# Optimization experiments

Hardware: AMD Instinct MI355X
Metric: run time of the kernel (lower is better)

## Reference

```python
import jax, jax.numpy as jnp
import numpy as np

LEVELS = 256          # 8-bit fake quant, quant_levels=256 in forward
SLM_CUTOFF = 0.05     # lower bound of the SLM LUT (file-loaded in original)
EPS = 1e-8


def _stats(t, pct):
    # QuantizeStats first-calibration-step semantics:
    # max = percentile(t, pct); min = t.min() if >= 0 else -max
    mx = jnp.percentile(t, pct)
    mn = jnp.min(t)
    mn = jnp.where(mn >= 0.0, mn, -mx)
    return jax.lax.stop_gradient(mn), jax.lax.stop_gradient(mx)


def _fake_quant_det(x, mn, mx, lut_min=None):
    diff = mx - mn
    q = jnp.clip(x, mn, mx)
    q = (q - mn) / (diff + EPS) * (LEVELS - 1)
    q = jnp.round(q) / (LEVELS - 1) * diff + mn
    if lut_min is not None:
        # clip positive part up to lut_min*max, negative part down to -lut_min*|min|
        pos = jax.nn.relu(q)
        neg = q - pos
        lms_p = lut_min * mx
        pos = jnp.where(pos < lms_p, lms_p, pos)
        lms_n = lut_min * jnp.abs(mn)
        neg = jnp.where(neg > -lms_n, -lms_n, neg)
        q = pos + neg
    # straight-through estimator (QuantizeValue.backward passes grad through)
    return x + jax.lax.stop_gradient(q - x)


def _fake_quant_rand(x, mn, mx, key):
    diff = mx - mn
    q = jnp.clip(x, mn, mx)
    q = (q - mn) / (diff + EPS) * (LEVELS - 1)
    noise = jax.random.uniform(key, q.shape, q.dtype) - 0.5  # stochastic rounding
    q = jnp.round(q + noise) / (LEVELS - 1) * diff + mn
    return x + jax.lax.stop_gradient(q - x)


def setup_inputs() -> dict:
    key = jax.random.key(0)
    kx, ky = jax.random.split(key)
    x = jax.random.normal(kx, (2, 4, 2048, 64), dtype=jnp.float32)
    y = jax.random.normal(ky, (2, 4, 64, 2048), dtype=jnp.float32)
    return {"x": x, "y": y}


def reference(x, y):
    # QuantizedMatmul.forward, quantize=True, training path
    x_min, x_max = _stats(x, 99.99)
    y_min, y_max = _stats(y, 98.0)
    xq = _fake_quant_det(x, x_min, x_max)
    yq = _fake_quant_det(y, y_min, y_max, SLM_CUTOFF)
    out = jnp.matmul(xq, yq)           # [B,H,M,N]
    o_min, o_max = _stats(out, 99.9999)
    return _fake_quant_rand(out, o_min, o_max, jax.random.key(1))
```

## Files before the change

### kernel.cpp

```cpp
#include <hip/hip_runtime.h>
#include <math.h>

#define CAP  (1u<<20)
#define LCAP 12288
#define LBUF 4096

typedef __attribute__((ext_vector_type(4))) float f32x4;
typedef __attribute__((ext_vector_type(8))) __bf16 bf16x8;
typedef __attribute__((ext_vector_type(8))) unsigned short u16x8;
typedef __attribute__((ext_vector_type(4))) unsigned short u16x4;

__device__ __forceinline__ unsigned f2key(float f){
  unsigned u = __float_as_uint(f);
  return (u & 0x80000000u) ? ~u : (u | 0x80000000u);
}
__device__ __forceinline__ float key2f(unsigned k){
  unsigned u = (k & 0x80000000u) ? (k & 0x7fffffffu) : ~k;
  return __uint_as_float(u);
}
__device__ __forceinline__ unsigned short f2bf(float f){
  unsigned u = __float_as_uint(f);
  u += 0x7FFFu + ((u>>16)&1u);
  return (unsigned short)(u>>16);
}

__device__ __forceinline__ void stage_bf16_tiles(
    const unsigned short* __restrict__ xq, const unsigned short* __restrict__ yqT,
    unsigned short* As, unsigned short* Bs, int brow, int bcol, int tid){
  #pragma unroll
  for (int i=0;i<4;i++){
    int u = tid + i*256;
    int row = u >> 3, ko = (u & 7) << 3;
    u16x8 v = *(const u16x8*)&xq[(size_t)(brow+row)*64 + ko];
    unsigned slot = ((unsigned)(ko>>3)) ^ ((unsigned)row & 7u);
    *(u16x8*)&As[(unsigned)row*64u + slot*8u] = v;
  }
  #pragma unroll
  for (int i=0;i<4;i++){
    int u = tid + i*256;
    int col = u >> 3, ko = (u & 7) << 3;
    u16x8 v = *(const u16x8*)&yqT[(size_t)(bcol+col)*64 + ko];
    unsigned slot = ((unsigned)(ko>>3)) ^ ((unsigned)col & 7u);
    *(u16x8*)&Bs[(unsigned)col*64u + slot*8u] = v;
  }
}

__device__ __forceinline__ void mfma_tile(
    const unsigned short* As, const unsigned short* Bs,
    f32x4 acc[2][8], int w, int lr, int lg){
  #pragma unroll
  for (int kk=0; kk<2; ++kk){
    bf16x8 a[2], bb[8];
    #pragma unroll
    for (int rt=0;rt<2;rt++){
      int row = w*32 + rt*16 + lr;
      unsigned slot = (unsigned)(kk*4 + lg) ^ ((unsigned)row & 7u);
      a[rt] = __builtin_bit_cast(bf16x8, *(const u16x8*)&As[(unsigned)row*64u + slot*8u]);
    }
    #pragma unroll
    for (int ct=0;ct<8;ct++){
      int col = ct*16 + lr;
      unsigned slot = (unsigned)(kk*4 + lg) ^ ((unsigned)col & 7u);
      bb[ct] = __builtin_bit_cast(bf16x8, *(const u16x8*)&Bs[(unsigned)col*64u + slot*8u]);
    }
    #pragma unroll
    for (int rt=0;rt<2;rt++)
      #pragma unroll
      for (int ct=0;ct<8;ct++)
        acc[rt][ct] = __builtin_amdgcn_mfma_f32_16x16x32_bf16(a[rt], bb[ct], acc[rt][ct], 0, 0, 0);
  }
}

__global__ void init_kernel(unsigned* ctrl){
  int tid = blockIdx.x*blockDim.x + threadIdx.x;
  int stride = gridDim.x*blockDim.x;
  for (int i=tid;i<8192;i+=stride) ctrl[i]=0u;
  if (tid<16) ctrl[12291+tid]=0u;
  if (tid>=16 && tid<19) ctrl[12288+(tid-16)]=0xFFFFFFFFu;
}

__global__ __launch_bounds__(256) void hist2_kernel(
    const float4* __restrict__ dA, const float4* __restrict__ dB, int n4A, int n4B,
    unsigned* __restrict__ hA, unsigned* __restrict__ hB,
    unsigned* __restrict__ mkA, unsigned* __restrict__ mkB){
  const int z = blockIdx.y;
  const float4* __restrict__ data = z ? dB : dA;
  const int n4 = z ? n4B : n4A;
  unsigned* hist = z ? hB : hA;
  unsigned* minKey = z ? mkB : mkA;
  __shared__ unsigned sh[8*4096];
  int tid = threadIdx.x;
  for (int i=tid;i<8*4096;i+=blockDim.x) sh[i]=0u;
  __syncthreads();
  const unsigned p = (unsigned)(tid & 7);
  const unsigned cp = p << 12;
  const unsigned rot = p << 2;
  unsigned lmin=0xFFFFFFFFu;
  int idx = blockIdx.x*blockDim.x + tid;
  int stride = gridDim.x*blockDim.x;
  for (int i=idx;i<n4;i+=stride){
    float4 v = data[i];
    unsigned k0=f2key(v.x), k1=f2key(v.y), k2=f2key(v.z), k3=f2key(v.w);
    atomicAdd(&sh[cp + (((k0>>20)+rot)&4095u)],1u);
    atomicAdd(&sh[cp + (((k1>>20)+rot)&4095u)],1u);
    atomicAdd(&sh[cp + (((k2>>20)+rot)&4095u)],1u);
    atomicAdd(&sh[cp + (((k3>>20)+rot)&4095u)],1u);
    lmin = min(lmin, min(min(k0,k1),min(k2,k3)));
  }
  #pragma unroll
  for (int off=32; off; off>>=1) lmin = min(lmin, __shfl_xor(lmin, off));
  if ((tid&63)==0) atomicMin(minKey, lmin);
  __syncthreads();
  for (int i=tid;i<4096;i+=blockDim.x){
    unsigned c=0;
    #pragma unroll
    for (int q=0;q<8;q++) c += sh[(q<<12) + (((unsigned)i + (q<<2))&4095u)];
    if(c) atomicAdd(&hist[i],c);
  }
}

__global__ __launch_bounds__(256) void collect2_kernel(
    const float4* __restrict__ dA, const float4* __restrict__ dB, int n4A, int n4B,
    const unsigned* __restrict__ hA, const unsigned* __restrict__ hB,
    unsigned k1A, unsigned k2A, unsigned k1B, unsigned k2B,
    float* __restrict__ candA, float* __restrict__ candB,
    unsigned* __restrict__ cntA, unsigned* __restrict__ cntB){
  const int z = blockIdx.y;
  const float4* __restrict__ data = z ? dB : dA;
  const int n4 = z ? n4B : n4A;
  const unsigned* __restrict__ hist = z ? hB : hA;
  const unsigned k1 = z ? k1B : k1A;
  const unsigned k2 = z ? k2B : k2A;
  float* cand = z ? candB : candA;
  unsigned* cnt = z ? cntB : cntA;
  __shared__ float sc[LBUF];
  __shared__ unsigned part[256];
  __shared__ unsigned sBi[2];
  __shared__ unsigned scnt, sbase;
  const int t = threadIdx.x;
  if (t==0) scnt=0u;
  unsigned h[16]; unsigned s=0;
  #pragma unroll
  for (int i=0;i<16;i++){ h[i] = hist[t*16+i]; s += h[i]; }
  part[t] = s;
  __syncthreads();
  for (int off=1; off<256; off<<=1){
    unsigned add = (t+off<256) ? part[t+off] : 0u;
    __syncthreads();
    part[t] += add;
    __syncthreads();
  }
  unsigned cum = (t<255) ? part[t+1] : 0u;
  for (int i=15;i>=0;--i){
    unsigned hh = h[i];
    unsigned b = (unsigned)(t*16+i);
    if (cum < k1 && cum + hh >= k1){ sBi[1] = b; }
    if (cum < k2 && cum + hh >= k2){ sBi[0] = b; }
    cum += hh;
  }
  __syncthreads();
  const unsigned blo = sBi[0], bhi = sBi[1];
  int idx = blockIdx.x*blockDim.x + t;
  int stride = gridDim.x*blockDim.x;
  for (int i=idx;i<n4;i+=stride){
    float4 v = data[i];
    float r[4] = {v.x,v.y,v.z,v.w};
    #pragma unroll
    for (int j=0;j<4;j++){
      unsigned b = f2key(r[j]) >> 20;
      if (b>=blo && b<=bhi){
        unsigned p = atomicAdd(&scnt,1u);
        if (p < LBUF) sc[p] = r[j];
        else { unsigned g = atomicAdd(cnt,1u); if (g<CAP) cand[g]=r[j]; }
      }
    }
  }
  __syncthreads();
  unsigned c = scnt; if (c > LBUF) c = LBUF;
  if (t==0 && c>0) sbase = atomicAdd(cnt, c);
  __syncthreads();
  for (unsigned i=t; i<c; i+=256){
    unsigned g = sbase + i;
    if (g < CAP) cand[g] = sc[i];
  }
}

__global__ __launch_bounds__(1024) void select2_kernel(
    const float* __restrict__ candA, const float* __restrict__ candB,
    const unsigned* __restrict__ cntA, const unsigned* __restrict__ cntB,
    const unsigned* __restrict__ hA, const unsigned* __restrict__ hB,
    const unsigned* __restrict__ mkA, const unsigned* __restrict__ mkB,
    unsigned k1A, unsigned k2A, unsigned k1B, unsigned k2B,
    double fracA, double fracB,
    float* __restrict__ stA, float* __restrict__ stB){
  const int z = blockIdx.x;
  const float* __restrict__ cand = z ? candB : candA;
  const unsigned* cnt = z ? cntB : cntA;
  const unsigned* __restrict__ hist_g = z ? hB : hA;
  const unsigned* mk  = z ? mkB  : mkA;
  const unsigned k1 = z ? k1B : k1A;
  const unsigned k2 = z ? k2B : k2A;
  const double frac = z ? fracB : fracA;
  float* stats = z ? stB : stA;

  __shared__ unsigned keys[LCAP];
  __shared__ unsigned histP[16*258];
  __shared__ unsigned hist[256];
  __shared__ unsigned part[256];
  __shared__ unsigned sAbove;
  __shared__ unsigned sPrefix, sK;
  __shared__ unsigned sKey[2];
  const int t = threadIdx.x;
  unsigned m = *cnt; if (m > CAP) m = CAP;
  for (unsigned i=t; i<m && i<LCAP; i+=1024) keys[i] = f2key(cand[i]);

  if (t==0) sAbove = 0u;
  if (hist_g){
    unsigned h[16]; unsigned s=0;
    if (t<256){
      #pragma unroll
      for (int i=0;i<16;i++){ h[i] = hist_g[t*16+i]; s += h[i]; }
      part[t] = s;
    }
    __syncthreads();
    for (int off=1; off<256; off<<=1){
      unsigned add = (t<256 && t+off<256) ? part[t+off] : 0u;
      __syncthreads();
      if (t<256) part[t] += add;
      __syncthreads();
    }
    if (t<256){
      unsigned cum = (t<255) ? part[t+1] : 0u;
      for (int i=15;i>=0;--i){
        unsigned hh = h[i];
        if (cum < k1 && cum + hh >= k1){ sAbove = cum; }
        cum += hh;
      }
    }
  }
  __syncthreads();
  const unsigned above = sAbove;

  for (int tg=0; tg<2; ++tg){
    unsigned k = ((tg==0) ? k1 : k2) - above;
    unsigned prefix = 0u, pmask = 0u;
    for (int s=24; s>=0; s-=8){
      for (int i=t;i<16*258;i+=1024) histP[i]=0u;
      __syncthreads();
      const unsigned base = (unsigned)(t & 15) * 258u;
      for (unsigned i=t;i<m;i+=1024){
        unsigned key = (i<LCAP) ? keys[i] : f2key(cand[i]);
        if ((key & pmask) == prefix) atomicAdd(&histP[base + ((key>>s)&255u)],1u);
      }
      __syncthreads();
      if (t<256){
        unsigned c=0;
        #pragma unroll
        for (int q=0;q<16;q++) c += histP[(unsigned)q*258u + (unsigned)t];
        hist[t] = c;
      }
      __syncthreads();
      if (t<64){
        unsigned h0=hist[t*4+0], h1=hist[t*4+1], h2=hist[t*4+2], h3=hist[t*4+3];
        unsigned g = h0+h1+h2+h3;
        unsigned acc = g;
        #pragma unroll
        for (int off=1; off<64; off<<=1){
          unsigned v = __shfl_down(acc, off);
          acc += (t+off<64) ? v : 0u;
        }
        unsigned ca3 = acc - g;
        unsigned ca2 = ca3 + h3;
        unsigned ca1 = ca2 + h2;
        unsigned ca0 = ca1 + h1;
        if (ca3<k && ca3+h3>=k){ sPrefix = prefix | ((unsigned)(4*t+3)<<s); sK = k-ca3; }
        if (ca2<k && ca2+h2>=k){ sPrefix = prefix | ((unsigned)(4*t+2)<<s); sK = k-ca2; }
        if (ca1<k && ca1+h1>=k){ sPrefix = prefix | ((unsigned)(4*t+1)<<s); sK = k-ca1; }
        if (ca0<k && ca0+h0>=k){ sPrefix = prefix | ((unsigned)(4*t+0)<<s); sK = k-ca0; }
      }
      __syncthreads();
      prefix = sPrefix;
      pmask |= (255u << s);
      k = sK;
    }
    if (t==0) sKey[tg] = prefix;
    __syncthreads();
  }
  if (t==0){
    float vhi = key2f(sKey[0]);
    float vlo = key2f(sKey[1]);
    double mx = (double)vlo + frac * ((double)vhi - (double)vlo);
    float mxf = (float)mx;
    float mnraw = key2f(*mk);
    float mnf = (mnraw >= 0.0f) ? mnraw : -mxf;
    stats[0]=mnf; stats[1]=mxf;
  }
}

__global__ __launch_bounds__(256) void prep_quant_kernel(
    const float4* __restrict__ x, const float* __restrict__ y,
    unsigned short* __restrict__ xq, unsigned short* __restrict__ yqT,
    int n4x, const float* __restrict__ stA, const float* __restrict__ stB){
  if (blockIdx.y == 0){
    const float amn=stA[0], amx=stA[1];
    const float adiff=amx-amn, adenom=adiff+1e-8f;
    int idx = blockIdx.x*256 + threadIdx.x;
    int stride = gridDim.x*256;
    for (int i=idx; i<n4x; i+=stride){
      float4 v = x[i];
      float rr[4]={v.x,v.y,v.z,v.w};
      u16x4 qv;
      #pragma unroll
      for (int j=0;j<4;j++){
        float xv = rr[j];
        float q = fminf(fmaxf(xv, amn), amx);
        q = (q - amn) / adenom * 255.0f;
        q = rintf(q);
        q = q / 255.0f * adiff + amn;
        qv[j] = f2bf(xv + (q - xv));
      }
      *(u16x4*)&xq[(size_t)i*4] = qv;
    }
  } else {
    __shared__ unsigned short Ys[64*72];
    const float bmn=stB[0], bmx=stB[1];
    const float bdiff=bmx-bmn, bdenom=bdiff+1e-8f;
    const float blp=0.05f*bmx, bln=0.05f*fabsf(bmn);
    const int blk = blockIdx.x;
    const int b = blk >> 5, ctile = blk & 31;
    const float* Y = y + (size_t)b*64*2048 + ctile*64;
    const int t = threadIdx.x;
    #pragma unroll
    for (int i=0;i<4;i++){
      int u = t + i*256;
      int k = u >> 4;
      int c4 = (u & 15) << 2;
      float4 v = *(const float4*)&Y[(size_t)k*2048 + c4];
      float rr[4]={v.x,v.y,v.z,v.w};
      #pragma unroll
      for (int j=0;j<4;j++){
        float xv = rr[j];
        float q = fminf(fmaxf(xv, bmn), bmx);
        q = (q - bmn) / bdenom * 255.0f;
        q = rintf(q);
        q = q / 255.0f * bdiff + bmn;
        float pos = fmaxf(q, 0.0f);
        float neg = q - pos;
        pos = (pos < blp) ? blp : pos;
        neg = (neg > -bln) ? -bln : neg;
        q = pos + neg;
        Ys[(c4+j)*72 + k] = f2bf(xv + (q - xv));
      }
    }
    __syncthreads();
    #pragma unroll
    for (int i=0;i<2;i++){
      int u = t + i*256;
      int col = u >> 3, ko = (u & 7) << 3;
      u16x8 v = *(const u16x8*)&Ys[col*72 + ko];
      *(u16x8*)&yqT[((size_t)b*2048 + ctile*64 + col)*64 + ko] = v;
    }
  }
}

__global__ __launch_bounds__(256) void matmul_stats_kernel(
    const unsigned short* __restrict__ xq, const unsigned short* __restrict__ yqT,
    unsigned* __restrict__ bMaxKey, unsigned* __restrict__ bMinKey){
  __shared__ unsigned short As[128*64];
  __shared__ unsigned short Bs[128*64];
  __shared__ float wred[8];
  const int b = blockIdx.z;
  const unsigned short* xqb  = xq  + (size_t)b*2048*64;
  const unsigned short* yqTb = yqT + (size_t)b*2048*64;
  const int brow = blockIdx.y*128, bcol = blockIdx.x*128;
  const int tid = threadIdx.x;
  stage_bf16_tiles(xqb, yqTb, As, Bs, brow, bcol, tid);
  __syncthreads();
  const int w = tid >> 6, l = tid & 63, lr = l & 15, lg = l >> 4;
  f32x4 zero = {0.f,0.f,0.f,0.f};
  f32x4 acc[2][8];
  #pragma unroll
  for (int rt=0;rt<2;rt++)
    #pragma unroll
    for (int ct=0;ct<8;ct++) acc[rt][ct]=zero;
  mfma_tile(As, Bs, acc, w, lr, lg);
  float tmx = -3.4e38f, tmn = 3.4e38f;
  #pragma unroll
  for (int rt=0;rt<2;rt++)
    #pragma unroll
    for (int ct=0;ct<8;ct++)
      #pragma unroll
      for (int g=0; g<4; g++){
        float v = acc[rt][ct][g];
        tmx = fmaxf(tmx, v);
        tmn = fminf(tmn, v);
      }
  #pragma unroll
  for (int off=32; off; off>>=1){
    tmx = fmaxf(tmx, __shfl_xor(tmx, off));
    tmn = fminf(tmn, __shfl_xor(tmn, off));
  }
  if ((tid&63)==0){ wred[tid>>6]=tmx; wred[4+(tid>>6)]=tmn; }
  __syncthreads();
  if (tid==0){
    float m4 = fmaxf(fmaxf(wred[0],wred[1]),fmaxf(wred[2],wred[3]));
    float n4 = fminf(fminf(wred[4],wred[5]),fminf(wred[6],wred[7]));
    int bid = blockIdx.x + (blockIdx.y<<4) + (blockIdx.z<<8);
    bMaxKey[bid] = f2key(m4);
    bMinKey[bid] = f2key(n4);
  }
}

__global__ __launch_bounds__(256) void thresh_kernel(
    const unsigned* __restrict__ bMaxKey, const unsigned* __restrict__ bMinKey,
    unsigned kth, unsigned* __restrict__ tkey, unsigned* __restrict__ minKeyO){
  __shared__ unsigned red[8];
  const int t = threadIdx.x;
  unsigned kz[8];
  unsigned mn = 0xFFFFFFFFu;
  #pragma unroll
  for (int i=0;i<8;i++){ kz[i] = bMaxKey[t*8+i]; mn = min(mn, bMinKey[t*8+i]); }
  #pragma unroll
  for (int off=32; off; off>>=1) mn = min(mn, __shfl_xor(mn, off));
  if ((t&63)==0) red[4+(t>>6)] = mn;
  __syncthreads();
  if (t==0) *minKeyO = min(min(red[4],red[5]),min(red[6],red[7]));
  unsigned lo=0u, hi=0xFFFFFFFFu;
  while (lo < hi){
    unsigned mid = lo + ((hi-lo)>>1) + 1u;
    unsigned c = 0;
    #pragma unroll
    for (int i=0;i<8;i++) c += (kz[i] >= mid) ? 1u : 0u;
    #pragma unroll
    for (int off=32; off; off>>=1) c += __shfl_xor(c, off);
    __syncthreads();
    if ((t&63)==0) red[t>>6] = c;
    __syncthreads();
    unsigned tot = red[0]+red[1]+red[2]+red[3];
    if (tot >= kth) lo = mid; else hi = mid - 1u;
  }
  if (t==0) *tkey = lo;
}

__global__ __launch_bounds__(256) void collect_tile_kernel(
    const unsigned short* __restrict__ xq, const unsigned short* __restrict__ yqT,
    const unsigned* __restrict__ bMaxKey, const unsigned* __restrict__ tkey,
    float* __restrict__ cand, unsigned* __restrict__ cnt){
  const unsigned T = *tkey;
  const int bid = blockIdx.x + (blockIdx.y<<4) + (blockIdx.z<<8);
  if (bMaxKey[bid] < T) return;
  __shared__ unsigned short As[128*64];
  __shared__ unsigned short Bs[128*64];
  __shared__ float sc[LBUF];
  __shared__ unsigned scnt, sbase;
  const int b = blockIdx.z;
  const unsigned short* xqb  = xq  + (size_t)b*2048*64;
  const unsigned short* yqTb = yqT + (size_t)b*2048*64;
  const int brow = blockIdx.y*128, bcol = blockIdx.x*128;
  const int tid = threadIdx.x;
  if (tid==0) scnt=0u;
  stage_bf16_tiles(xqb, yqTb, As, Bs, brow, bcol, tid);
  __syncthreads();
  const int w = tid >> 6, l = tid & 63, lr = l & 15, lg = l >> 4;
  f32x4 zero = {0.f,0.f,0.f,0.f};
  f32x4 acc[2][8];
  #pragma unroll
  for (int rt=0;rt<2;rt++)
    #pragma unroll
    for (int ct=0;ct<8;ct++) acc[rt][ct]=zero;
  mfma_tile(As, Bs, acc, w, lr, lg);
  #pragma unroll
  for (int rt=0;rt<2;rt++)
    #pragma unroll
    for (int ct=0;ct<8;ct++)
      #pragma unroll
      for (int g=0; g<4; g++){
        float v = acc[rt][ct][g];
        if (f2key(v) >= T){
          unsigned p = atomicAdd(&scnt,1u);
          if (p < LBUF) sc[p] = v;
          else { unsigned gg = atomicAdd(cnt,1u); if (gg<CAP) cand[gg]=v; }
        }
      }
  __syncthreads();
  unsigned c = scnt; if (c > LBUF) c = LBUF;
  if (tid==0 && c>0) sbase = atomicAdd(cnt, c);
  __syncthreads();
  for (unsigned i=tid; i<c; i+=256){
    unsigned g = sbase + i;
    if (g < CAP) cand[g] = sc[i];
  }
}

__global__ __launch_bounds__(256) void matmul_quant_kernel(
    const unsigned short* __restrict__ xq, const unsigned short* __restrict__ yqT,
    float* __restrict__ C, const float* __restrict__ stO){
  __shared__ float smem[8704];
  unsigned short* As = (unsigned short*)smem;
  unsigned short* Bs = As + 8192;
  const float omn=stO[0], omx=stO[1];
  const float odiff=omx-omn, odenom=odiff+1e-8f;
  const int b = blockIdx.z;
  const unsigned short* xqb  = xq  + (size_t)b*2048*64;
  const unsigned short* yqTb = yqT + (size_t)b*2048*64;
  C += (size_t)b*2048*2048;
  const int brow = blockIdx.y*128, bcol = blockIdx.x*128;
  const int tid = threadIdx.x;
  stage_bf16_tiles(xqb, yqTb, As, Bs, brow, bcol, tid);
  __syncthreads();
  const int w = tid >> 6, l = tid & 63, lr = l & 15, lg = l >> 4;
  f32x4 zero = {0.f,0.f,0.f,0.f};
  f32x4 acc[2][8];
  #pragma unroll
  for (int rt=0;rt<2;rt++)
    #pragma unroll
    for (int ct=0;ct<8;ct++) acc[rt][ct]=zero;
  mfma_tile(As, Bs, acc, w, lr, lg);
  __syncthreads();
  float* Cw = smem + w*2176;
  #pragma unroll
  for (int h=0; h<2; ++h){
    #pragma unroll
    for (int rt=0;rt<2;rt++)
      #pragma unroll
      for (int c2=0;c2<4;c2++){
        int ct = h*4 + c2;
        #pragma unroll
        for (int g=0; g<4; g++){
          float x = acc[rt][ct][g];
          float q = fminf(fmaxf(x, omn), omx);
          q = (q - omn) / odenom * 255.0f;
          q = rintf(q);
          q = q / 255.0f * odiff + omn;
          Cw[(rt*16 + lg*4 + g)*68 + c2*16 + lr] = x + (q - x);
        }
      }
    #pragma unroll
    for (int i=0;i<8;i++){
      int u = l + 64*i;
      int row = u >> 4;
      int c4 = (u & 15) << 2;
      float4 v4 = *(float4*)&Cw[row*68 + c4];
      int gr = brow + w*32 + row;
      *(float4*)&C[(size_t)gr*2048 + bcol + h*64 + c4] = v4;
    }
  }
}

static void percentile_ranks(long long n, double pct, unsigned& k1, unsigned& k2, double& frac){
  double p = (double)(n - 1) * (pct / 100.0);
  double fi = floor(p);
  frac = p - fi;
  long long i0 = (long long)fi;
  k2 = (unsigned)(n - i0);
  k1 = k2 - 1u;
}

extern "C" void kernel_launch(void* const* d_in, const int* in_sizes, int n_in,
                              void* d_out, int out_size, void* d_ws, size_t ws_size,
                              hipStream_t stream) {
  const float* x = (const float*)d_in[0];
  const float* y = (const float*)d_in[1];
  float* out = (float*)d_out;
  char* ws = (char*)d_ws;

  const long long nX = (long long)in_sizes[0];
  const long long nY = (long long)in_sizes[1];
  const long long nO = (long long)out_size;
  const int nX4 = (int)(nX/4), nY4 = (int)(nY/4);

  float*    candx = (float*)(ws);
  float*    candy = (float*)(ws + (5ll<<20));
  float*    cando = (float*)(ws + (10ll<<20));
  unsigned* ctrl  = (unsigned*)(ws + (15ll<<20));
  unsigned short* xq  = (unsigned short*)(ws + (16ll<<20));
  unsigned short* yqT = (unsigned short*)(ws + (18ll<<20));
  unsigned *hx = ctrl, *hy = ctrl+4096;
  unsigned* minkey = ctrl + 12288;
  unsigned* cnt    = ctrl + 12291;
  unsigned* tkey   = ctrl + 12303;
  float* stx = (float*)(ctrl + 12304);
  float* sty = stx + 2;
  float* sto = stx + 4;
  unsigned* bMaxKey = ctrl + 12320;
  unsigned* bMinKey = ctrl + 14368;

  unsigned k1x,k2x,k1y,k2y,k1o,k2o; double fx,fy,fo;
  percentile_ranks(nX, 99.99,   k1x, k2x, fx);
  percentile_ranks(nY, 98.0,    k1y, k2y, fy);
  percentile_ranks(nO, 99.9999, k1o, k2o, fo);

  init_kernel<<<32,256,0,stream>>>(ctrl);

  hist2_kernel<<<dim3(128,2),256,0,stream>>>((const float4*)x,(const float4*)y,nX4,nY4,hx,hy,minkey+0,minkey+1);
  collect2_kernel<<<dim3(128,2),256,0,stream>>>((const float4*)x,(const float4*)y,nX4,nY4,hx,hy,
                                                k1x,k2x,k1y,k2y,candx,candy,cnt+0,cnt+1);
  select2_kernel<<<2,1024,0,stream>>>(candx,candy,cnt+0,cnt+1,hx,hy,minkey+0,minkey+1,
                                      k1x,k2x,k1y,k2y,fx,fy,stx,sty);

  prep_quant_kernel<<<dim3(256,2),256,0,stream>>>((const float4*)x, y, xq, yqT, nX4, stx, sty);

  matmul_stats_kernel<<<dim3(16,16,8),256,0,stream>>>(xq, yqT, bMaxKey, bMinKey);

  thresh_kernel<<<1,256,0,stream>>>(bMaxKey, bMinKey, k2o, tkey, minkey+2);
  collect_tile_kernel<<<dim3(16,16,8),256,0,stream>>>(xq, yqT, bMaxKey, tkey, cando, cnt+2);
  select2_kernel<<<1,1024,0,stream>>>(cando,cando,cnt+2,cnt+2,(const unsigned*)nullptr,(const unsigned*)nullptr,
                                      minkey+2,minkey+2,k1o,k2o,k1o,k2o,fo,fo,sto,sto);

  matmul_quant_kernel<<<dim3(16,16,8),256,0,stream>>>(xq, yqT, out, sto);
}
```

Baseline: 138.9 us.

## Fold threshold and output select into last-block tails of matmul kernels

The separate thresh_kernel and output select2_kernel launches are removed. Their work now runs in the last block to finish matmul_stats_kernel and collect_tile_kernel, detected with a global done counter and threadfence plus atomic loads. Candidates are stored as sortable keys, and the radix select runs in 256 threads inside the collect kernel. The final quant epilogue also drops its LDS transpose and writes scalars straight to global memory. This saves two kernel launches, but the tail work runs serially in a single block, and the uncoalesced stores may cost bandwidth. The select2 hist_g null check is also removed, so that path now always reads hist_g.

Result: slower. 206.2 us (+48.4%).

```diff
diff --git a/kernel.cpp b/kernel.cpp
--- a/kernel.cpp
+++ b/kernel.cpp
@@ -23,6 +23,7 @@
   u += 0x7FFFu + ((u>>16)&1u);
   return (unsigned short)(u>>16);
 }
+__device__ __forceinline__ unsigned aload(unsigned* p){ return atomicOr(p, 0u); }
 
 __device__ __forceinline__ void stage_bf16_tiles(
     const unsigned short* __restrict__ xq, const unsigned short* __restrict__ yqT,
@@ -215,7 +216,7 @@
   for (unsigned i=t; i<m && i<LCAP; i+=1024) keys[i] = f2key(cand[i]);
 
   if (t==0) sAbove = 0u;
-  if (hist_g){
+  {
     unsigned h[16]; unsigned s=0;
     if (t<256){
       #pragma unroll
@@ -365,10 +366,13 @@
 
 __global__ __launch_bounds__(256) void matmul_stats_kernel(
     const unsigned short* __restrict__ xq, const unsigned short* __restrict__ yqT,
-    unsigned* __restrict__ bMaxKey, unsigned* __restrict__ bMinKey){
+    unsigned* bMaxKey, unsigned* bMinKey,
+    unsigned* doneS, unsigned kth, unsigned* tkey, unsigned* minKeyO){
   __shared__ unsigned short As[128*64];
   __shared__ unsigned short Bs[128*64];
   __shared__ float wred[8];
+  __shared__ unsigned red[8];
+  __shared__ int sLast;
   const int b = blockIdx.z;
   const unsigned short* xqb  = xq  + (size_t)b*2048*64;
   const unsigned short* yqTb = yqT + (size_t)b*2048*64;
@@ -406,98 +410,173 @@
     float m4 = fmaxf(fmaxf(wred[0],wred[1]),fmaxf(wred[2],wred[3]));
     float n4 = fminf(fminf(wred[4],wred[5]),fminf(wred[6],wred[7]));
     int bid = blockIdx.x + (blockIdx.y<<4) + (blockIdx.z<<8);
-    bMaxKey[bid] = f2key(m4);
-    bMinKey[bid] = f2key(n4);
-  }
-}
-
-__global__ __launch_bounds__(256) void thresh_kernel(
-    const unsigned* __restrict__ bMaxKey, const unsigned* __restrict__ bMinKey,
-    unsigned kth, unsigned* __restrict__ tkey, unsigned* __restrict__ minKeyO){
-  __shared__ unsigned red[8];
-  const int t = threadIdx.x;
-  unsigned kz[8];
-  unsigned mn = 0xFFFFFFFFu;
-  #pragma unroll
-  for (int i=0;i<8;i++){ kz[i] = bMaxKey[t*8+i]; mn = min(mn, bMinKey[t*8+i]); }
-  #pragma unroll
-  for (int off=32; off; off>>=1) mn = min(mn, __shfl_xor(mn, off));
-  if ((t&63)==0) red[4+(t>>6)] = mn;
-  __syncthreads();
-  if (t==0) *minKeyO = min(min(red[4],red[5]),min(red[6],red[7]));
-  unsigned lo=0u, hi=0xFFFFFFFFu;
-  while (lo < hi){
-    unsigned mid = lo + ((hi-lo)>>1) + 1u;
-    unsigned c = 0;
-    #pragma unroll
-    for (int i=0;i<8;i++) c += (kz[i] >= mid) ? 1u : 0u;
-    #pragma unroll
-    for (int off=32; off; off>>=1) c += __shfl_xor(c, off);
-    __syncthreads();
-    if ((t&63)==0) red[t>>6] = c;
-    __syncthreads();
-    unsigned tot = red[0]+red[1]+red[2]+red[3];
-    if (tot >= kth) lo = mid; else hi = mid - 1u;
-  }
-  if (t==0) *tkey = lo;
+    atomicExch(&bMaxKey[bid], f2key(m4));
+    atomicExch(&bMinKey[bid], f2key(n4));
+    __threadfence();
+    unsigned old = atomicAdd(doneS, 1u);
+    sLast = (old == 2047u);
+  }
+  __syncthreads();
+  if (sLast){
+    unsigned kz[8];
+    unsigned mn = 0xFFFFFFFFu;
+    #pragma unroll
+    for (int i=0;i<8;i++){ kz[i] = aload(&bMaxKey[tid*8+i]); mn = min(mn, aload(&bMinKey[tid*8+i])); }
+    #pragma unroll
+    for (int off=32; off; off>>=1) mn = min(mn, __shfl_xor(mn, off));
+    if ((tid&63)==0) red[4+(tid>>6)] = mn;
+    __syncthreads();
+    if (tid==0) *minKeyO = min(min(red[4],red[5]),min(red[6],red[7]));
+    unsigned lo=0u, hi=0xFFFFFFFFu;
+    while (lo < hi){
+      unsigned mid = lo + ((hi-lo)>>1) + 1u;
+      unsigned c = 0;
+      #pragma unroll
+      for (int i=0;i<8;i++) c += (kz[i] >= mid) ? 1u : 0u;
+      #pragma unroll
+      for (int off=32; off; off>>=1) c += __shfl_xor(c, off);
+      __syncthreads();
+      if ((tid&63)==0) red[tid>>6] = c;
+      __syncthreads();
+      unsigned tot = red[0]+red[1]+red[2]+red[3];
+      if (tot >= kth) lo = mid; else hi = mid - 1u;
+    }
+    if (tid==0) *tkey = lo;
+  }
 }
 
 __global__ __launch_bounds__(256) void collect_tile_kernel(
     const unsigned short* __restrict__ xq, const unsigned short* __restrict__ yqT,
     const unsigned* __restrict__ bMaxKey, const unsigned* __restrict__ tkey,
-    float* __restrict__ cand, unsigned* __restrict__ cnt){
+    unsigned* cand, unsigned* cnt, unsigned* doneC,
+    const unsigned* __restrict__ minKeyO,
+    unsigned k1o, unsigned k2o, double fo, float* stO){
+  __shared__ unsigned S[12544];
+  __shared__ unsigned scnt, sbase;
+  __shared__ int sLast;
+  __shared__ unsigned sPrefix, sK, sKeyv[2];
   const unsigned T = *tkey;
   const int bid = blockIdx.x + (blockIdx.y<<4) + (blockIdx.z<<8);
-  if (bMaxKey[bid] < T) return;
-  __shared__ unsigned short As[128*64];
-  __shared__ unsigned short Bs[128*64];
-  __shared__ float sc[LBUF];
-  __shared__ unsigned scnt, sbase;
-  const int b = blockIdx.z;
-  const unsigned short* xqb  = xq  + (size_t)b*2048*64;
-  const unsigned short* yqTb = yqT + (size_t)b*2048*64;
-  const int brow = blockIdx.y*128, bcol = blockIdx.x*128;
   const int tid = threadIdx.x;
   if (tid==0) scnt=0u;
-  stage_bf16_tiles(xqb, yqTb, As, Bs, brow, bcol, tid);
-  __syncthreads();
-  const int w = tid >> 6, l = tid & 63, lr = l & 15, lg = l >> 4;
-  f32x4 zero = {0.f,0.f,0.f,0.f};
-  f32x4 acc[2][8];
-  #pragma unroll
-  for (int rt=0;rt<2;rt++)
-    #pragma unroll
-    for (int ct=0;ct<8;ct++) acc[rt][ct]=zero;
-  mfma_tile(As, Bs, acc, w, lr, lg);
-  #pragma unroll
-  for (int rt=0;rt<2;rt++)
-    #pragma unroll
-    for (int ct=0;ct<8;ct++)
-      #pragma unroll
-      for (int g=0; g<4; g++){
-        float v = acc[rt][ct][g];
-        if (f2key(v) >= T){
-          unsigned p = atomicAdd(&scnt,1u);
-          if (p < LBUF) sc[p] = v;
-          else { unsigned gg = atomicAdd(cnt,1u); if (gg<CAP) cand[gg]=v; }
+  __syncthreads();
+  if (bMaxKey[bid] >= T){
+    unsigned short* As = (unsigned short*)S;
+    unsigned short* Bs = (unsigned short*)(S + 4096);
+    unsigned* scU = S + 8192;
+    const int b = blockIdx.z;
+    const unsigned short* xqb  = xq  + (size_t)b*2048*64;
+    const unsigned short* yqTb = yqT + (size_t)b*2048*64;
+    const int brow = blockIdx.y*128, bcol = blockIdx.x*128;
+    stage_bf16_tiles(xqb, yqTb, As, Bs, brow, bcol, tid);
+    __syncthreads();
+    const int w = tid >> 6, l = tid & 63, lr = l & 15, lg = l >> 4;
+    f32x4 zero = {0.f,0.f,0.f,0.f};
+    f32x4 acc[2][8];
+    #pragma unroll
+    for (int rt=0;rt<2;rt++)
+      #pragma unroll
+      for (int ct=0;ct<8;ct++) acc[rt][ct]=zero;
+    mfma_tile(As, Bs, acc, w, lr, lg);
+    #pragma unroll
+    for (int rt=0;rt<2;rt++)
+      #pragma unroll
+      for (int ct=0;ct<8;ct++)
+        #pragma unroll
+        for (int g=0; g<4; g++){
+          unsigned key = f2key(acc[rt][ct][g]);
+          if (key >= T){
+            unsigned p = atomicAdd(&scnt,1u);
+            if (p < LBUF) scU[p] = key;
+            else { unsigned gg = atomicAdd(cnt,1u); if (gg<CAP) atomicExch(&cand[gg], key); }
+          }
         }
-      }
-  __syncthreads();
-  unsigned c = scnt; if (c > LBUF) c = LBUF;
-  if (tid==0 && c>0) sbase = atomicAdd(cnt, c);
-  __syncthreads();
-  for (unsigned i=tid; i<c; i+=256){
-    unsigned g = sbase + i;
-    if (g < CAP) cand[g] = sc[i];
+    __syncthreads();
+    unsigned c = scnt; if (c > LBUF) c = LBUF;
+    if (tid==0 && c>0) sbase = atomicAdd(cnt, c);
+    __syncthreads();
+    for (unsigned i=tid; i<c; i+=256){
+      unsigned g = sbase + i;
+      if (g < CAP) atomicExch(&cand[g], scU[i]);
+    }
+  }
+  __syncthreads();
+  if (tid==0){
+    __threadfence();
+    unsigned old = atomicAdd(doneC, 1u);
+    sLast = (old == 2047u);
+  }
+  __syncthreads();
+  if (sLast){
+    unsigned* keys  = S;
+    unsigned* histP = S + 4096;
+    unsigned* hist  = S + 8208;
+    unsigned m = aload(cnt); if (m > CAP) m = CAP;
+    for (unsigned i=tid; i<m && i<4096u; i+=256) keys[i] = aload(&cand[i]);
+    __syncthreads();
+    for (int tg=0; tg<2; ++tg){
+      unsigned k = (tg==0) ? k1o : k2o;
+      unsigned prefix = 0u, pmask = 0u;
+      for (int s=24; s>=0; s-=8){
+        for (int i=tid;i<16*257;i+=256) histP[i]=0u;
+        __syncthreads();
+        const unsigned base = (unsigned)(tid & 15) * 257u;
+        for (unsigned i=tid;i<m;i+=256){
+          unsigned key = (i<4096u) ? keys[i] : aload(&cand[i]);
+          if ((key & pmask) == prefix) atomicAdd(&histP[base + ((key>>s)&255u)],1u);
+        }
+        __syncthreads();
+        {
+          unsigned c=0;
+          #pragma unroll
+          for (int q=0;q<16;q++) c += histP[(unsigned)q*257u + (unsigned)tid];
+          hist[tid] = c;
+        }
+        __syncthreads();
+        if (tid<64){
+          unsigned h0=hist[tid*4+0], h1=hist[tid*4+1], h2=hist[tid*4+2], h3=hist[tid*4+3];
+          unsigned g = h0+h1+h2+h3;
+          unsigned acc2 = g;
+          #pragma unroll
+          for (int off=1; off<64; off<<=1){
+            unsigned v = __shfl_down(acc2, off);
+            acc2 += (tid+off<64) ? v : 0u;
+          }
+          unsigned ca3 = acc2 - g;
+          unsigned ca2 = ca3 + h3;
+          unsigned ca1 = ca2 + h2;
+          unsigned ca0 = ca1 + h1;
+          if (ca3<k && ca3+h3>=k){ sPrefix = prefix | ((unsigned)(4*tid+3)<<s); sK = k-ca3; }
+          if (ca2<k && ca2+h2>=k){ sPrefix = prefix | ((unsigned)(4*tid+2)<<s); sK = k-ca2; }
+          if (ca1<k && ca1+h1>=k){ sPrefix = prefix | ((unsigned)(4*tid+1)<<s); sK = k-ca1; }
+          if (ca0<k && ca0+h0>=k){ sPrefix = prefix | ((unsigned)(4*tid+0)<<s); sK = k-ca0; }
+        }
+        __syncthreads();
+        prefix = sPrefix;
+        pmask |= (255u << s);
+        k = sK;
+        __syncthreads();
+      }
+      if (tid==0) sKeyv[tg] = prefix;
+      __syncthreads();
+    }
+    if (tid==0){
+      float vhi = key2f(sKeyv[0]);
+      float vlo = key2f(sKeyv[1]);
+      double mx = (double)vlo + fo * ((double)vhi - (double)vlo);
+      float mxf = (float)mx;
+      float mnraw = key2f(*minKeyO);
+      float mnf = (mnraw >= 0.0f) ? mnraw : -mxf;
+      stO[0]=mnf; stO[1]=mxf;
+    }
   }
 }
 
 __global__ __launch_bounds__(256) void matmul_quant_kernel(
     const unsigned short* __restrict__ xq, const unsigned short* __restrict__ yqT,
     float* __restrict__ C, const float* __restrict__ stO){
-  __shared__ float smem[8704];
-  unsigned short* As = (unsigned short*)smem;
-  unsigned short* Bs = As + 8192;
+  __shared__ unsigned short As[128*64];
+  __shared__ unsigned short Bs[128*64];
   const float omn=stO[0], omx=stO[1];
   const float odiff=omx-omn, odenom=odiff+1e-8f;
   const int b = blockIdx.z;
@@ -516,35 +595,22 @@
     #pragma unroll
     for (int ct=0;ct<8;ct++) acc[rt][ct]=zero;
   mfma_tile(As, Bs, acc, w, lr, lg);
-  __syncthreads();
-  float* Cw = smem + w*2176;
-  #pragma unroll
-  for (int h=0; h<2; ++h){
-    #pragma unroll
-    for (int rt=0;rt<2;rt++)
-      #pragma unroll
-      for (int c2=0;c2<4;c2++){
-        int ct = h*4 + c2;
-        #pragma unroll
-        for (int g=0; g<4; g++){
-          float x = acc[rt][ct][g];
-          float q = fminf(fmaxf(x, omn), omx);
-          q = (q - omn) / odenom * 255.0f;
-          q = rintf(q);
-          q = q / 255.0f * odiff + omn;
-          Cw[(rt*16 + lg*4 + g)*68 + c2*16 + lr] = x + (q - x);
-        }
-      }
-    #pragma unroll
-    for (int i=0;i<8;i++){
-      int u = l + 64*i;
-      int row = u >> 4;
-      int c4 = (u & 15) << 2;
-      float4 v4 = *(float4*)&Cw[row*68 + c4];
-      int gr = brow + w*32 + row;
-      *(float4*)&C[(size_t)gr*2048 + bcol + h*64 + c4] = v4;
-    }
-  }
+  #pragma unroll
+  for (int rt=0;rt<2;rt++)
+    #pragma unroll
+    for (int ct=0;ct<8;ct++)
+      #pragma unroll
+      for (int g=0; g<4; g++){
+        float x = acc[rt][ct][g];
+        float q = fminf(fmaxf(x, omn), omx);
+        q = (q - omn) / odenom * 255.0f;
+        q = rintf(q);
+        q = q / 255.0f * odiff + omn;
+        float v = x + (q - x);
+        int row = brow + w*32 + rt*16 + lg*4 + g;
+        int col = bcol + ct*16 + lr;
+        C[(size_t)row*2048 + col] = v;
+      }
 }
 
 static void percentile_ranks(long long n, double pct, unsigned& k1, unsigned& k2, double& frac){
@@ -571,13 +637,15 @@
 
   float*    candx = (float*)(ws);
   float*    candy = (float*)(ws + (5ll<<20));
-  float*    cando = (float*)(ws + (10ll<<20));
+  unsigned* cando = (unsigned*)(ws + (10ll<<20));
   unsigned* ctrl  = (unsigned*)(ws + (15ll<<20));
   unsigned short* xq  = (unsigned short*)(ws + (16ll<<20));
   unsigned short* yqT = (unsigned short*)(ws + (18ll<<20));
   unsigned *hx = ctrl, *hy = ctrl+4096;
   unsigned* minkey = ctrl + 12288;
   unsigned* cnt    = ctrl + 12291;
+  unsigned* doneS  = ctrl + 12296;
+  unsigned* doneC  = ctrl + 12297;
   unsigned* tkey   = ctrl + 12303;
   float* stx = (float*)(ctrl + 12304);
   float* sty = stx + 2;
@@ -600,12 +668,12 @@
 
   prep_quant_kernel<<<dim3(256,2),256,0,stream>>>((const float4*)x, y, xq, yqT, nX4, stx, sty);
 
-  matmul_stats_kernel<<<dim3(16,16,8),256,0,stream>>>(xq, yqT, bMaxKey, bMinKey);
-
-  thresh_kernel<<<1,256,0,stream>>>(bMaxKey, bMinKey, k2o, tkey, minkey+2);
-  collect_tile_kernel<<<dim3(16,16,8),256,0,stream>>>(xq, yqT, bMaxKey, tkey, cando, cnt+2);
-  select2_kernel<<<1,1024,0,stream>>>(cando,cando,cnt+2,cnt+2,(const unsigned*)nullptr,(const unsigned*)nullptr,
-                                      minkey+2,minkey+2,k1o,k2o,k1o,k2o,fo,fo,sto,sto);
+  matmul_stats_kernel<<<dim3(16,16,8),256,0,stream>>>(xq, yqT, bMaxKey, bMinKey,
+                                                      doneS, k2o, tkey, minkey+2);
+
+  collect_tile_kernel<<<dim3(16,16,8),256,0,stream>>>(xq, yqT, bMaxKey, tkey,
+                                                      cando, cnt+2, doneC, minkey+2,
+                                                      k1o, k2o, fo, sto);
 
   matmul_quant_kernel<<<dim3(16,16,8),256,0,stream>>>(xq, yqT, out, sto);
 }
```
